# Optimization experiments

Measured on AMD Instinct MI355X. Metric: run time of the kernel, lower is better.

## Reference

```python
import jax, jax.numpy as jnp
import numpy as np


def setup_inputs() -> dict:
    key = jax.random.key(0)
    k1, k2, k3 = jax.random.split(key, 3)
    B, H, S, D = 2, 16, 2048, 64
    return {
        "q": jax.random.normal(k1, (B, H, S, D), dtype=jnp.float32),
        "k": jax.random.normal(k2, (B, H, S, D), dtype=jnp.float32),
        "v": jax.random.normal(k3, (B, H, S, D), dtype=jnp.float32),
        "chunk_size": 256,
    }


def reference(q, k, v, chunk_size):
    # Chunked Based linear attention: linear (K^T V) + rank-3 quadratic (K x K x V)
    # inter-chunk state recurrence (shifted/exclusive cumsum over chunks) plus the
    # intra-chunk causal part with kernel  s = q.k;  phi = s + 0.5*s^2.
    B, H, S, D = q.shape
    C = chunk_size
    N = S // C
    scale = D ** (-0.5)

    qc = (q * scale).reshape(B, H, N, C, D)
    kc = k.reshape(B, H, N, C, D)
    vc = v.reshape(B, H, N, C, D)

    # ---- linear inter-chunk state: shifted cumsum of K^T V per chunk ----
    KV = jnp.einsum("bhncd,bhnce->bhnde", kc, vc)            # (B,H,N,D,D)
    S_lin = jnp.cumsum(KV, axis=2) - KV                       # exclusive cumsum
    o_lin = jnp.einsum("bhncd,bhnde->bhnce", qc, S_lin)

    # ---- quadratic inter-chunk state: shifted cumsum of sum_c K_d K_e V_f ----
    KKV = jnp.einsum("bhncd,bhnce,bhncf->bhndef", kc, kc, vc)  # (B,H,N,D,D,D)
    S_quad = jnp.cumsum(KKV, axis=2) - KKV                     # exclusive cumsum
    o_quad = 0.5 * jnp.einsum("bhndef,bhncd,bhnce->bhncf", S_quad, qc, qc)

    # ---- intra-chunk causal quadratic attention ----
    A = jnp.einsum("bhncd,bhnmd->bhncm", qc, kc)               # (B,H,N,C,C)
    mask = jnp.tril(jnp.ones((C, C), dtype=bool))
    Ak = jnp.where(mask, A + 0.5 * A * A, 0.0)
    o_intra = jnp.einsum("bhncm,bhnmf->bhncf", Ak, vc)

    out = (o_lin + o_quad + o_intra).reshape(B, H, S, D)
    return out
```

## Files before the change

kernel.cpp:

```cpp
#include <hip/hip_runtime.h>
#include <stdint.h>

#define SEQ  2048
#define DH   64
#define BH_N 32
#define SCALE 0.125f

typedef __attribute__((ext_vector_type(8))) short short8;
typedef __attribute__((ext_vector_type(4))) float f32x4;

static __device__ __forceinline__ unsigned short f2bf(float f) {
  unsigned int u = __float_as_uint(f);
  u += 0x7fffu + ((u >> 16) & 1u);
  return (unsigned short)(u >> 16);
}
static __device__ __forceinline__ unsigned cvtpk(float a, float b) {
  unsigned r;
  asm("v_cvt_pk_bf16_f32 %0, %1, %2" : "=v"(r) : "v"(a), "v"(b));
  return r;
}

typedef __attribute__((address_space(1))) const unsigned char* gp1;
typedef __attribute__((address_space(3))) unsigned char* lp3;
static __device__ __forceinline__ void stage16(const void* g, void* l) {
  __builtin_amdgcn_global_load_lds((gp1)g, (lp3)l, 16, 0, 0);
}

__global__ __launch_bounds__(256) void prep_kernel(
    const float* __restrict__ kin, const float* __restrict__ vin,
    unsigned short* __restrict__ kb2, unsigned short* __restrict__ vt2)
{
  const int sb = blockIdx.x;
  const int bh = blockIdx.y;
  const int t  = threadIdx.x;
  __shared__ __align__(16) unsigned short lds[4096];
  const size_t base  = ((size_t)bh * SEQ + (size_t)sb * 64) * DH;
  const size_t obase = ((size_t)bh * 32 + sb) * 4096;

  #pragma unroll
  for (int i = 0; i < 4; ++i) {
    int idx = i * 256 + t, key = idx >> 4, F = (idx & 15) * 4;
    float4 f = *reinterpret_cast<const float4*>(kin + base + key * DH + F);
    int pos = (key & 32) | ((key & 4) << 2) | ((key & 24) >> 1) | (key & 3);
    int c = (F >> 5) * 4 + ((F >> 3) & 3), jh = (F >> 2) & 1;
    uint2 pk; pk.x = cvtpk(f.x, f.y); pk.y = cvtpk(f.z, f.w);
    *reinterpret_cast<uint2*>(lds + (c * 64 + pos) * 8 + jh * 4) = pk;
  }
  __syncthreads();
  #pragma unroll
  for (int uu = 0; uu < 2; ++uu) {
    int u = uu * 256 + t;
    *reinterpret_cast<uint4*>(kb2 + obase + u * 8) =
        *reinterpret_cast<const uint4*>(lds + u * 8);
  }
  __syncthreads();
  #pragma unroll
  for (int i = 0; i < 4; ++i) {
    int idx = i * 256 + t, key = idx >> 4, F = (idx & 15) * 4;
    float4 f = *reinterpret_cast<const float4*>(vin + base + key * DH + F);
    int a = key >> 5, qd = (key >> 3) & 3, jj = key & 7;
    int u0 = a * 256 + (F >> 4) * 64 + qd * 16 + (F & 15);
    lds[(u0 + 0) * 8 + jj] = f2bf(f.x);
    lds[(u0 + 1) * 8 + jj] = f2bf(f.y);
    lds[(u0 + 2) * 8 + jj] = f2bf(f.z);
    lds[(u0 + 3) * 8 + jj] = f2bf(f.w);
  }
  __syncthreads();
  #pragma unroll
  for (int uu = 0; uu < 2; ++uu) {
    int u = uu * 256 + t;
    *reinterpret_cast<uint4*>(vt2 + obase + u * 8) =
        *reinterpret_cast<const uint4*>(lds + u * 8);
  }
}

__global__ __launch_bounds__(256, 2) void attn_kernel(
    const float* __restrict__ q,
    const unsigned short* __restrict__ kb2,
    const unsigned short* __restrict__ vt2,
    float* __restrict__ out)
{
  const int lid  = blockIdx.y * 16 + blockIdx.x;
  const int xcd  = lid & 7;
  const int jj_  = lid >> 3;
  const int bh   = (xcd << 2) | (jj_ >> 4);
  const int qa   = jj_ & 15;
  const int tid  = threadIdx.x;
  const int w    = tid >> 6;
  const int lane = tid & 63;
  const int low  = lane & 15;
  const int quad = lane >> 4;
  const int p    = w >> 1;
  const int rh   = w & 1;
  const int nB   = 32 - qa;

  __shared__ __align__(16) unsigned short kls[2][2][4096];
  __shared__ __align__(16) unsigned short vls[2][2][4096];

  const unsigned short* kb_h = kb2 + (size_t)bh * 32 * 4096;
  const unsigned short* v2_h = vt2 + (size_t)bh * 32 * 4096;

  short8 aqA[2][2], aqB[2][2];
  #pragma unroll
  for (int tsel = 0; tsel < 2; ++tsel) {
    const int qt = tsel ? (31 - qa) : qa;
    #pragma unroll
    for (int h = 0; h < 2; ++h) {
      const float* qp =
          q + ((size_t)bh * SEQ + qt * 64 + rh * 32 + h * 16 + low) * DH + quad * 8;
      #pragma unroll
      for (int ks = 0; ks < 2; ++ks) {
        float4 f0 = *reinterpret_cast<const float4*>(qp + ks * 32);
        float4 f1 = *reinterpret_cast<const float4*>(qp + ks * 32 + 4);
        uint4 uv;
        uv.x = cvtpk(f0.x * SCALE, f0.y * SCALE);
        uv.y = cvtpk(f0.z * SCALE, f0.w * SCALE);
        uv.z = cvtpk(f1.x * SCALE, f1.y * SCALE);
        uv.w = cvtpk(f1.z * SCALE, f1.w * SCALE);
        short8 a = __builtin_bit_cast(short8, uv);
        if (tsel) aqB[h][ks] = a; else aqA[h][ks] = a;
      }
    }
  }

  f32x4 oaccA[2][4], oaccB[2][4];
  #pragma unroll
  for (int h = 0; h < 2; ++h)
    #pragma unroll
    for (int i = 0; i < 4; ++i) {
      oaccA[h][i] = (f32x4){0.f, 0.f, 0.f, 0.f};
      oaccB[h][i] = (f32x4){0.f, 0.f, 0.f, 0.f};
    }

  const int slot = w & 1;
  const unsigned short* gsrc = (w >> 1) ? v2_h : kb_h;
  unsigned short* ldst0 = (w >> 1) ? &vls[0][slot][0] : &kls[0][slot][0];
  unsigned short* ldst1 = (w >> 1) ? &vls[1][slot][0] : &kls[1][slot][0];

  #define STAGE(I, B)                                                          \
    do {                                                                       \
      int s_ = 2 * (I) + slot; if (s_ > 32) s_ = 32;                           \
      const int T_ = (s_ < nB) ? s_ : (s_ - nB);                               \
      const unsigned short* gs_ = gsrc + (size_t)T_ * 4096;                    \
      unsigned short* ld_ = (B) ? ldst1 : ldst0;                               \
      _Pragma("unroll")                                                        \
      for (int r_ = 0; r_ < 8; ++r_)                                           \
        stage16(gs_ + (r_ * 64 + lane) * 8, ld_ + (r_ * 64 + lane) * 8);       \
    } while (0)

  #define COMPUTE(AQ, OACC)                                                    \
    do {                                                                       \
      _Pragma("unroll")                                                        \
      for (int a = 0; a < 2; ++a) {                                            \
        short8 vfa[4];                                                         \
        _Pragma("unroll")                                                      \
        for (int ft = 0; ft < 4; ++ft)                                         \
          vfa[ft] = *reinterpret_cast<const short8*>(                          \
              vT + ((a * 4 + ft) * 64 + lane) * 8);                            \
        f32x4 s00 = (f32x4){0.f, 0.f, 0.f, 0.f};                               \
        f32x4 s01 = s00, s10 = s00, s11 = s00;                                 \
        _Pragma("unroll")                                                      \
        for (int ks = 0; ks < 2; ++ks) {                                       \
          short8 kf0 = *reinterpret_cast<const short8*>(                       \
              kT + ((ks * 4 + quad) * 64 + (a * 2 + 0) * 16 + low) * 8);       \
          short8 kf1 = *reinterpret_cast<const short8*>(                       \
              kT + ((ks * 4 + quad) * 64 + (a * 2 + 1) * 16 + low) * 8);       \
          s00 = __builtin_amdgcn_mfma_f32_16x16x32_bf16(kf0, AQ[0][ks], s00, 0, 0, 0); \
          s01 = __builtin_amdgcn_mfma_f32_16x16x32_bf16(kf0, AQ[1][ks], s01, 0, 0, 0); \
          s10 = __builtin_amdgcn_mfma_f32_16x16x32_bf16(kf1, AQ[0][ks], s10, 0, 0, 0); \
          s11 = __builtin_amdgcn_mfma_f32_16x16x32_bf16(kf1, AQ[1][ks], s11, 0, 0, 0); \
        }                                                                      \
        _Pragma("unroll")                                                      \
        for (int h = 0; h < 2; ++h) {                                          \
          f32x4 sA = h ? s01 : s00;           \
          f32x4 sB = h ? s11 : s10;           \
          float pv[8];                                                         \
          _Pragma("unroll")                                                    \
          for (int r = 0; r < 4; ++r) {                                        \
            float x0 = sA[r], x1 = sB[r];                                      \
            pv[r]     = __builtin_fmaf(0.5f * x0, x0, x0);                     \
            pv[4 + r] = __builtin_fmaf(0.5f * x1, x1, x1);                     \
          }                                                                    \
          if (diag) {                                                          \
            const int qrow = rh * 32 + h * 16 + low;                           \
            _Pragma("unroll")                                                  \
            for (int r = 0; r < 4; ++r) {                                      \
              if ((a * 32 + quad * 8 + r) > qrow)     pv[r]     = 0.f;         \
              if ((a * 32 + quad * 8 + 4 + r) > qrow) pv[4 + r] = 0.f;         \
            }                                                                  \
          }                                                                    \
          uint4 uu;                                                            \
          uu.x = cvtpk(pv[0], pv[1]); uu.y = cvtpk(pv[2], pv[3]);              \
          uu.z = cvtpk(pv[4], pv[5]); uu.w = cvtpk(pv[6], pv[7]);              \
          short8 pf = __builtin_bit_cast(short8, uu);                          \
          _Pragma("unroll")                                                    \
          for (int ft = 0; ft < 4; ++ft)                                       \
            OACC[h][ft] = __builtin_amdgcn_mfma_f32_16x16x32_bf16(             \
                vfa[ft], pf, OACC[h][ft], 0, 0, 0);                            \
        }                                                                      \
      }                                                                        \
    } while (0)

  STAGE(0, 0);

  for (int i = 0; i < 17; ++i) {
    const int b = i & 1;
    __builtin_amdgcn_s_barrier();
    if (i < 16) {
      STAGE(i + 1, b ^ 1);
      asm volatile("s_waitcnt vmcnt(8)" ::: "memory");
    } else {
      asm volatile("s_waitcnt vmcnt(0)" ::: "memory");
    }
    __builtin_amdgcn_s_barrier();
    asm volatile("" ::: "memory");

    const int s = 2 * i + p;
    if (s > 32) continue;
    const bool diag = (s == nB - 1) || (s == 32);
    const unsigned short* kT = &kls[b][p][0];
    const unsigned short* vT = &vls[b][p][0];

    if (s >= nB) COMPUTE(aqA, oaccA);
    else         COMPUTE(aqB, oaccB);
  }

  __syncthreads();
  float* mb = reinterpret_cast<float*>(&kls[0][0][0]);
  float* mw = mb + rh * 4096;
  if (p == 1) {
    #pragma unroll
    for (int h = 0; h < 2; ++h)
      #pragma unroll
      for (int ft = 0; ft < 4; ++ft) {
        *reinterpret_cast<f32x4*>(mw + ((0 * 8 + h * 4 + ft) * 256 + lane * 4)) =
            oaccA[h][ft];
        *reinterpret_cast<f32x4*>(mw + ((1 * 8 + h * 4 + ft) * 256 + lane * 4)) =
            oaccB[h][ft];
      }
  }
  __syncthreads();
  if (p == 0) {
    #pragma unroll
    for (int tsel = 0; tsel < 2; ++tsel) {
      const int qt = tsel ? (31 - qa) : qa;
      #pragma unroll
      for (int h = 0; h < 2; ++h)
        #pragma unroll
        for (int ft = 0; ft < 4; ++ft) {
          f32x4 o = tsel ? oaccB[h][ft] : oaccA[h][ft];
          f32x4 m = *reinterpret_cast<const f32x4*>(
              mw + ((tsel * 8 + h * 4 + ft) * 256 + lane * 4));
          o += m;
          *reinterpret_cast<f32x4*>(
              out + ((size_t)bh * SEQ + qt * 64 + rh * 32 + h * 16 + low) * DH +
              ft * 16 + quad * 4) = o;
        }
    }
  }
}

extern "C" void kernel_launch(void* const* d_in, const int* in_sizes, int n_in,
                              void* d_out, int out_size, void* d_ws, size_t ws_size,
                              hipStream_t stream)
{
  const float* q = (const float*)d_in[0];
  const float* k = (const float*)d_in[1];
  const float* v = (const float*)d_in[2];
  float* out = (float*)d_out;

  unsigned short* kb2 = (unsigned short*)d_ws;
  unsigned short* vt2 = kb2 + (size_t)BH_N * SEQ * DH;

  prep_kernel<<<dim3(32, BH_N), 256, 0, stream>>>(k, v, kb2, vt2);
  attn_kernel<<<dim3(16, BH_N), 256, 0, stream>>>(q, kb2, vt2, out);
}
```

Measured before the change: 119.9 us.

## Split key-half work across 8 waves with 512-thread blocks and two-stage reduction

```diff
diff --git a/kernel.cpp b/kernel.cpp
--- a/kernel.cpp
+++ b/kernel.cpp
@@ -74,7 +74,7 @@
   }
 }
 
-__global__ __launch_bounds__(256, 2) void attn_kernel(
+__global__ __launch_bounds__(512, 4) void attn_kernel(
     const float* __restrict__ q,
     const unsigned short* __restrict__ kb2,
     const unsigned short* __restrict__ vt2,
@@ -90,8 +90,9 @@
   const int lane = tid & 63;
   const int low  = lane & 15;
   const int quad = lane >> 4;
-  const int p    = w >> 1;
-  const int rh   = w & 1;
+  const int p    = w & 1;
+  const int rh   = (w >> 1) & 1;
+  const int ah   = w >> 2;
   const int nB   = 32 - qa;
 
   __shared__ __align__(16) unsigned short kls[2][2][4096];
@@ -132,72 +133,74 @@
       oaccB[h][i] = (f32x4){0.f, 0.f, 0.f, 0.f};
     }
 
-  const int slot = w & 1;
-  const unsigned short* gsrc = (w >> 1) ? v2_h : kb_h;
-  unsigned short* ldst0 = (w >> 1) ? &vls[0][slot][0] : &kls[0][slot][0];
-  unsigned short* ldst1 = (w >> 1) ? &vls[1][slot][0] : &kls[1][slot][0];
+  const int tile_ = w >> 1;
+  const int sslot = tile_ & 1;
+  const bool stV  = (tile_ >> 1) != 0;
+  const int half_ = w & 1;
+  const unsigned short* gsrc = stV ? v2_h : kb_h;
+  unsigned short* ldst0 = stV ? &vls[0][sslot][0] : &kls[0][sslot][0];
+  unsigned short* ldst1 = stV ? &vls[1][sslot][0] : &kls[1][sslot][0];
 
   #define STAGE(I, B)                                                          \
     do {                                                                       \
-      int s_ = 2 * (I) + slot; if (s_ > 32) s_ = 32;                           \
+      int s_ = 2 * (I) + sslot; if (s_ > 32) s_ = 32;                          \
       const int T_ = (s_ < nB) ? s_ : (s_ - nB);                               \
       const unsigned short* gs_ = gsrc + (size_t)T_ * 4096;                    \
       unsigned short* ld_ = (B) ? ldst1 : ldst0;                               \
       _Pragma("unroll")                                                        \
-      for (int r_ = 0; r_ < 8; ++r_)                                           \
-        stage16(gs_ + (r_ * 64 + lane) * 8, ld_ + (r_ * 64 + lane) * 8);       \
+      for (int r_ = 0; r_ < 4; ++r_) {                                         \
+        const int rr_ = half_ * 4 + r_;                                        \
+        stage16(gs_ + (rr_ * 64 + lane) * 8, ld_ + (rr_ * 64 + lane) * 8);     \
+      }                                                                        \
     } while (0)
 
   #define COMPUTE(AQ, OACC)                                                    \
     do {                                                                       \
+      short8 vfa[4];                                                           \
       _Pragma("unroll")                                                        \
-      for (int a = 0; a < 2; ++a) {                                            \
-        short8 vfa[4];                                                         \
+      for (int ft = 0; ft < 4; ++ft)                                           \
+        vfa[ft] = *reinterpret_cast<const short8*>(                            \
+            vT + ((ah * 4 + ft) * 64 + lane) * 8);                             \
+      f32x4 s00 = (f32x4){0.f, 0.f, 0.f, 0.f};                                 \
+      f32x4 s01 = s00, s10 = s00, s11 = s00;                                   \
+      _Pragma("unroll")                                                        \
+      for (int ks = 0; ks < 2; ++ks) {                                         \
+        short8 kf0 = *reinterpret_cast<const short8*>(                         \
+            kT + ((ks * 4 + quad) * 64 + (ah * 2 + 0) * 16 + low) * 8);        \
+        short8 kf1 = *reinterpret_cast<const short8*>(                         \
+            kT + ((ks * 4 + quad) * 64 + (ah * 2 + 1) * 16 + low) * 8);        \
+        s00 = __builtin_amdgcn_mfma_f32_16x16x32_bf16(kf0, AQ[0][ks], s00, 0, 0, 0); \
+        s01 = __builtin_amdgcn_mfma_f32_16x16x32_bf16(kf0, AQ[1][ks], s01, 0, 0, 0); \
+        s10 = __builtin_amdgcn_mfma_f32_16x16x32_bf16(kf1, AQ[0][ks], s10, 0, 0, 0); \
+        s11 = __builtin_amdgcn_mfma_f32_16x16x32_bf16(kf1, AQ[1][ks], s11, 0, 0, 0); \
+      }                                                                        \
+      _Pragma("unroll")                                                        \
+      for (int h = 0; h < 2; ++h) {                                            \
+        f32x4 sA = h ? s01 : s00;                   \
+        f32x4 sB = h ? s11 : s10;                   \
+        float pv[8];                                                           \
+        _Pragma("unroll")                                                      \
+        for (int r = 0; r < 4; ++r) {                                          \
+          float x0 = sA[r], x1 = sB[r];                                        \
+          pv[r]     = __builtin_fmaf(0.5f * x0, x0, x0);                       \
+          pv[4 + r] = __builtin_fmaf(0.5f * x1, x1, x1);                       \
+        }                                                                      \
+        if (diag) {                                                            \
+          const int qrow = rh * 32 + h * 16 + low;                             \
+          _Pragma("unroll")                                                    \
+          for (int r = 0; r < 4; ++r) {                                        \
+            if ((ah * 32 + quad * 8 + r) > qrow)     pv[r]     = 0.f;          \
+            if ((ah * 32 + quad * 8 + 4 + r) > qrow) pv[4 + r] = 0.f;          \
+          }                                                                    \
+        }                                                                      \
+        uint4 uu;                                                              \
+        uu.x = cvtpk(pv[0], pv[1]); uu.y = cvtpk(pv[2], pv[3]);                \
+        uu.z = cvtpk(pv[4], pv[5]); uu.w = cvtpk(pv[6], pv[7]);                \
+        short8 pf = __builtin_bit_cast(short8, uu);                            \
         _Pragma("unroll")                                                      \
         for (int ft = 0; ft < 4; ++ft)                                         \
-          vfa[ft] = *reinterpret_cast<const short8*>(                          \
-              vT + ((a * 4 + ft) * 64 + lane) * 8);                            \
-        f32x4 s00 = (f32x4){0.f, 0.f, 0.f, 0.f};                               \
-        f32x4 s01 = s00, s10 = s00, s11 = s00;                                 \
-        _Pragma("unroll")                                                      \
-        for (int ks = 0; ks < 2; ++ks) {                                       \
-          short8 kf0 = *reinterpret_cast<const short8*>(                       \
-              kT + ((ks * 4 + quad) * 64 + (a * 2 + 0) * 16 + low) * 8);       \
-          short8 kf1 = *reinterpret_cast<const short8*>(                       \
-              kT + ((ks * 4 + quad) * 64 + (a * 2 + 1) * 16 + low) * 8);       \
-          s00 = __builtin_amdgcn_mfma_f32_16x16x32_bf16(kf0, AQ[0][ks], s00, 0, 0, 0); \
-          s01 = __builtin_amdgcn_mfma_f32_16x16x32_bf16(kf0, AQ[1][ks], s01, 0, 0, 0); \
-          s10 = __builtin_amdgcn_mfma_f32_16x16x32_bf16(kf1, AQ[0][ks], s10, 0, 0, 0); \
-          s11 = __builtin_amdgcn_mfma_f32_16x16x32_bf16(kf1, AQ[1][ks], s11, 0, 0, 0); \
-        }                                                                      \
-        _Pragma("unroll")                                                      \
-        for (int h = 0; h < 2; ++h) {                                          \
-          f32x4 sA = h ? s01 : s00;           \
-          f32x4 sB = h ? s11 : s10;           \
-          float pv[8];                                                         \
-          _Pragma("unroll")                                                    \
-          for (int r = 0; r < 4; ++r) {                                        \
-            float x0 = sA[r], x1 = sB[r];                                      \
-            pv[r]     = __builtin_fmaf(0.5f * x0, x0, x0);                     \
-            pv[4 + r] = __builtin_fmaf(0.5f * x1, x1, x1);                     \
-          }                                                                    \
-          if (diag) {                                                          \
-            const int qrow = rh * 32 + h * 16 + low;                           \
-            _Pragma("unroll")                                                  \
-            for (int r = 0; r < 4; ++r) {                                      \
-              if ((a * 32 + quad * 8 + r) > qrow)     pv[r]     = 0.f;         \
-              if ((a * 32 + quad * 8 + 4 + r) > qrow) pv[4 + r] = 0.f;         \
-            }                                                                  \
-          }                                                                    \
-          uint4 uu;                                                            \
-          uu.x = cvtpk(pv[0], pv[1]); uu.y = cvtpk(pv[2], pv[3]);              \
-          uu.z = cvtpk(pv[4], pv[5]); uu.w = cvtpk(pv[6], pv[7]);              \
-          short8 pf = __builtin_bit_cast(short8, uu);                          \
-          _Pragma("unroll")                                                    \
-          for (int ft = 0; ft < 4; ++ft)                                       \
-            OACC[h][ft] = __builtin_amdgcn_mfma_f32_16x16x32_bf16(             \
-                vfa[ft], pf, OACC[h][ft], 0, 0, 0);                            \
-        }                                                                      \
+          OACC[h][ft] = __builtin_amdgcn_mfma_f32_16x16x32_bf16(               \
+              vfa[ft], pf, OACC[h][ft], 0, 0, 0);                              \
       }                                                                        \
     } while (0)
 
@@ -208,7 +211,7 @@
     __builtin_amdgcn_s_barrier();
     if (i < 16) {
       STAGE(i + 1, b ^ 1);
-      asm volatile("s_waitcnt vmcnt(8)" ::: "memory");
+      asm volatile("s_waitcnt vmcnt(4)" ::: "memory");
     } else {
       asm volatile("s_waitcnt vmcnt(0)" ::: "memory");
     }
@@ -226,21 +229,51 @@
   }
 
   __syncthreads();
-  float* mb = reinterpret_cast<float*>(&kls[0][0][0]);
-  float* mw = mb + rh * 4096;
-  if (p == 1) {
-    #pragma unroll
-    for (int h = 0; h < 2; ++h)
-      #pragma unroll
-      for (int ft = 0; ft < 4; ++ft) {
-        *reinterpret_cast<f32x4*>(mw + ((0 * 8 + h * 4 + ft) * 256 + lane * 4)) =
-            oaccA[h][ft];
-        *reinterpret_cast<f32x4*>(mw + ((1 * 8 + h * 4 + ft) * 256 + lane * 4)) =
-            oaccB[h][ft];
-      }
-  }
-  __syncthreads();
-  if (p == 0) {
+  float* R00 = reinterpret_cast<float*>(&kls[0][0][0]);
+  float* R01 = reinterpret_cast<float*>(&kls[1][0][0]);
+  float* R10 = reinterpret_cast<float*>(&vls[0][0][0]);
+  float* R11 = reinterpret_cast<float*>(&vls[1][0][0]);
+  float* Rp = p ? (rh ? R11 : R10) : (rh ? R01 : R00);
+
+  if (ah == 1) {
+    #pragma unroll
+    for (int tsel = 0; tsel < 2; ++tsel)
+      #pragma unroll
+      for (int h = 0; h < 2; ++h)
+        #pragma unroll
+        for (int ft = 0; ft < 4; ++ft)
+          *reinterpret_cast<f32x4*>(
+              Rp + ((tsel * 8 + h * 4 + ft) * 256 + lane * 4)) =
+              tsel ? oaccB[h][ft] : oaccA[h][ft];
+  }
+  __syncthreads();
+  if (ah == 0) {
+    #pragma unroll
+    for (int tsel = 0; tsel < 2; ++tsel)
+      #pragma unroll
+      for (int h = 0; h < 2; ++h)
+        #pragma unroll
+        for (int ft = 0; ft < 4; ++ft) {
+          f32x4 m = *reinterpret_cast<const f32x4*>(
+              Rp + ((tsel * 8 + h * 4 + ft) * 256 + lane * 4));
+          if (tsel) oaccB[h][ft] += m; else oaccA[h][ft] += m;
+        }
+  }
+  __syncthreads();
+  float* Rr = rh ? R01 : R00;
+  if (ah == 0 && p == 1) {
+    #pragma unroll
+    for (int tsel = 0; tsel < 2; ++tsel)
+      #pragma unroll
+      for (int h = 0; h < 2; ++h)
+        #pragma unroll
+        for (int ft = 0; ft < 4; ++ft)
+          *reinterpret_cast<f32x4*>(
+              Rr + ((tsel * 8 + h * 4 + ft) * 256 + lane * 4)) =
+              tsel ? oaccB[h][ft] : oaccA[h][ft];
+  }
+  __syncthreads();
+  if (ah == 0 && p == 0) {
     #pragma unroll
     for (int tsel = 0; tsel < 2; ++tsel) {
       const int qt = tsel ? (31 - qa) : qa;
@@ -250,7 +283,7 @@
         for (int ft = 0; ft < 4; ++ft) {
           f32x4 o = tsel ? oaccB[h][ft] : oaccA[h][ft];
           f32x4 m = *reinterpret_cast<const f32x4*>(
-              mw + ((tsel * 8 + h * 4 + ft) * 256 + lane * 4));
+              Rr + ((tsel * 8 + h * 4 + ft) * 256 + lane * 4));
           o += m;
           *reinterpret_cast<f32x4*>(
               out + ((size_t)bh * SEQ + qt * 64 + rh * 32 + h * 16 + low) * DH +
@@ -273,5 +306,5 @@
   unsigned short* vt2 = kb2 + (size_t)BH_N * SEQ * DH;
 
   prep_kernel<<<dim3(32, BH_N), 256, 0, stream>>>(k, v, kb2, vt2);
-  attn_kernel<<<dim3(16, BH_N), 256, 0, stream>>>(q, kb2, vt2, out);
-}
+  attn_kernel<<<dim3(16, BH_N), 512, 0, stream>>>(q, kb2, vt2, out);
+}
```

Result: slower. 226.8 us (+89.2%).

## Read K/V tiles directly from global memory instead of LDS double-buffering

Applied to the files above, without the earlier changes.

```diff
diff --git a/kernel.cpp b/kernel.cpp
--- a/kernel.cpp
+++ b/kernel.cpp
@@ -18,12 +18,6 @@
   unsigned r;
   asm("v_cvt_pk_bf16_f32 %0, %1, %2" : "=v"(r) : "v"(a), "v"(b));
   return r;
-}
-
-typedef __attribute__((address_space(1))) const unsigned char* gp1;
-typedef __attribute__((address_space(3))) unsigned char* lp3;
-static __device__ __forceinline__ void stage16(const void* g, void* l) {
-  __builtin_amdgcn_global_load_lds((gp1)g, (lp3)l, 16, 0, 0);
 }
 
 __global__ __launch_bounds__(256) void prep_kernel(
@@ -94,8 +88,7 @@
   const int rh   = w & 1;
   const int nB   = 32 - qa;
 
-  __shared__ __align__(16) unsigned short kls[2][2][4096];
-  __shared__ __align__(16) unsigned short vls[2][2][4096];
+  __shared__ __align__(16) float mls[8192];
 
   const unsigned short* kb_h = kb2 + (size_t)bh * 32 * 4096;
   const unsigned short* v2_h = vt2 + (size_t)bh * 32 * 4096;
@@ -132,22 +125,6 @@
       oaccB[h][i] = (f32x4){0.f, 0.f, 0.f, 0.f};
     }
 
-  const int slot = w & 1;
-  const unsigned short* gsrc = (w >> 1) ? v2_h : kb_h;
-  unsigned short* ldst0 = (w >> 1) ? &vls[0][slot][0] : &kls[0][slot][0];
-  unsigned short* ldst1 = (w >> 1) ? &vls[1][slot][0] : &kls[1][slot][0];
-
-  #define STAGE(I, B)                                                          \
-    do {                                                                       \
-      int s_ = 2 * (I) + slot; if (s_ > 32) s_ = 32;                           \
-      const int T_ = (s_ < nB) ? s_ : (s_ - nB);                               \
-      const unsigned short* gs_ = gsrc + (size_t)T_ * 4096;                    \
-      unsigned short* ld_ = (B) ? ldst1 : ldst0;                               \
-      _Pragma("unroll")                                                        \
-      for (int r_ = 0; r_ < 8; ++r_)                                           \
-        stage16(gs_ + (r_ * 64 + lane) * 8, ld_ + (r_ * 64 + lane) * 8);       \
-    } while (0)
-
   #define COMPUTE(AQ, OACC)                                                    \
     do {                                                                       \
       _Pragma("unroll")                                                        \
@@ -156,15 +133,15 @@
         _Pragma("unroll")                                                      \
         for (int ft = 0; ft < 4; ++ft)                                         \
           vfa[ft] = *reinterpret_cast<const short8*>(                          \
-              vT + ((a * 4 + ft) * 64 + lane) * 8);                            \
+              vTg + ((a * 4 + ft) * 64 + lane) * 8);                           \
         f32x4 s00 = (f32x4){0.f, 0.f, 0.f, 0.f};                               \
         f32x4 s01 = s00, s10 = s00, s11 = s00;                                 \
         _Pragma("unroll")                                                      \
         for (int ks = 0; ks < 2; ++ks) {                                       \
           short8 kf0 = *reinterpret_cast<const short8*>(                       \
-              kT + ((ks * 4 + quad) * 64 + (a * 2 + 0) * 16 + low) * 8);       \
+              kTg + ((ks * 4 + quad) * 64 + (a * 2 + 0) * 16 + low) * 8);      \
           short8 kf1 = *reinterpret_cast<const short8*>(                       \
-              kT + ((ks * 4 + quad) * 64 + (a * 2 + 1) * 16 + low) * 8);       \
+              kTg + ((ks * 4 + quad) * 64 + (a * 2 + 1) * 16 + low) * 8);      \
           s00 = __builtin_amdgcn_mfma_f32_16x16x32_bf16(kf0, AQ[0][ks], s00, 0, 0, 0); \
           s01 = __builtin_amdgcn_mfma_f32_16x16x32_bf16(kf0, AQ[1][ks], s01, 0, 0, 0); \
           s10 = __builtin_amdgcn_mfma_f32_16x16x32_bf16(kf1, AQ[0][ks], s10, 0, 0, 0); \
@@ -172,8 +149,8 @@
         }                                                                      \
         _Pragma("unroll")                                                      \
         for (int h = 0; h < 2; ++h) {                                          \
-          f32x4 sA = h ? s01 : s00;           \
-          f32x4 sB = h ? s11 : s10;           \
+          f32x4 sA = h ? s01 : s00;                  \
+          f32x4 sB = h ? s11 : s10;                  \
           float pv[8];                                                         \
           _Pragma("unroll")                                                    \
           for (int r = 0; r < 4; ++r) {                                        \
@@ -201,33 +178,17 @@
       }                                                                        \
     } while (0)
 
-  STAGE(0, 0);
-
-  for (int i = 0; i < 17; ++i) {
-    const int b = i & 1;
-    __builtin_amdgcn_s_barrier();
-    if (i < 16) {
-      STAGE(i + 1, b ^ 1);
-      asm volatile("s_waitcnt vmcnt(8)" ::: "memory");
-    } else {
-      asm volatile("s_waitcnt vmcnt(0)" ::: "memory");
-    }
-    __builtin_amdgcn_s_barrier();
-    asm volatile("" ::: "memory");
-
-    const int s = 2 * i + p;
-    if (s > 32) continue;
+  for (int s = p; s <= 32; s += 2) {
     const bool diag = (s == nB - 1) || (s == 32);
-    const unsigned short* kT = &kls[b][p][0];
-    const unsigned short* vT = &vls[b][p][0];
-
+    const int T = (s < nB) ? s : (s - nB);
+    const unsigned short* kTg = kb_h + (size_t)T * 4096;
+    const unsigned short* vTg = v2_h + (size_t)T * 4096;
     if (s >= nB) COMPUTE(aqA, oaccA);
     else         COMPUTE(aqB, oaccB);
   }
 
   __syncthreads();
-  float* mb = reinterpret_cast<float*>(&kls[0][0][0]);
-  float* mw = mb + rh * 4096;
+  float* mw = mls + rh * 4096;
   if (p == 1) {
     #pragma unroll
     for (int h = 0; h < 2; ++h)
```

Result: slower. 132.8 us (+10.8%).
